# Optimization experiments

Measured on AMD Instinct MI355X. Metric: run time of the kernel, lower is better.

Reference implementation:

```python
import jax, jax.numpy as jnp
import numpy as np

D_MODEL = 256
D_FFN = 1024
N_LEVELS = 4
N_HEADS = 8
N_POINTS = 4
HEAD_DIM = D_MODEL // N_HEADS
SPATIAL = [(128, 128), (64, 64), (32, 32), (16, 16)]
LQ = sum(h * w for h, w in SPATIAL)  # 21760
B = 2


def setup_inputs() -> dict:
    key = jax.random.key(0)
    ks = jax.random.split(key, 24)

    def w(k, shape, s=0.02):
        return (jax.random.normal(k, shape) * s).astype(jnp.float32)

    HLP = N_HEADS * N_LEVELS * N_POINTS
    starts = np.cumsum([0] + [h * w_ for h, w_ in SPATIAL[:-1]])
    return {
        "src": jax.random.normal(ks[0], (B, LQ, D_MODEL), jnp.float32),
        "pos": 0.1 * jax.random.normal(ks[1], (B, LQ, D_MODEL), jnp.float32),
        "reference_points": jax.random.uniform(ks[2], (B, LQ, N_LEVELS, 2), jnp.float32),
        "W_off": w(ks[3], (D_MODEL, HLP * 2)),
        "b_off": w(ks[4], (HLP * 2,), 0.5),
        "W_attn": w(ks[5], (D_MODEL, HLP)),
        "b_attn": jnp.zeros((HLP,), jnp.float32),
        "W_val": w(ks[6], (D_MODEL, D_MODEL)),
        "b_val": jnp.zeros((D_MODEL,), jnp.float32),
        "W_out": w(ks[7], (D_MODEL, D_MODEL)),
        "b_out": jnp.zeros((D_MODEL,), jnp.float32),
        "ln1_g": jnp.ones((D_MODEL,), jnp.float32),
        "ln1_b": jnp.zeros((D_MODEL,), jnp.float32),
        "W1": w(ks[8], (D_MODEL, D_FFN)),
        "b1": jnp.zeros((D_FFN,), jnp.float32),
        "W2": w(ks[9], (D_FFN, D_MODEL)),
        "b2": jnp.zeros((D_MODEL,), jnp.float32),
        "ln2_g": jnp.ones((D_MODEL,), jnp.float32),
        "ln2_b": jnp.zeros((D_MODEL,), jnp.float32),
        "spatial_shapes": np.array(SPATIAL, np.int32),
        "level_start_index": np.array(starts, np.int32),
    }


def _layernorm(x, g, b):
    mu = x.mean(-1, keepdims=True)
    var = ((x - mu) ** 2).mean(-1, keepdims=True)
    return (x - mu) * jax.lax.rsqrt(var + 1e-5) * g + b


def _bilinear_sample(v, x, y, H, W):
    # v: [N, H, W, D]; x, y: [N, Lq, P] pixel coords (align_corners=False, zero pad)
    x0f = jnp.floor(x)
    y0f = jnp.floor(y)
    x0 = x0f.astype(jnp.int32)
    y0 = y0f.astype(jnp.int32)
    wx1 = x - x0f
    wy1 = y - y0f
    wx0 = 1.0 - wx1
    wy0 = 1.0 - wy1
    vf = v.reshape(v.shape[0], H * W, v.shape[-1])

    def gather(xi, yi, wt):
        valid = (xi >= 0) & (xi < W) & (yi >= 0) & (yi < H)
        idx = jnp.clip(yi, 0, H - 1) * W + jnp.clip(xi, 0, W - 1)
        g = jnp.take_along_axis(vf, idx.reshape(idx.shape[0], -1)[..., None], axis=1)
        g = g.reshape(*xi.shape, vf.shape[-1])
        return g * (wt * valid.astype(wt.dtype))[..., None]

    return (gather(x0, y0, wx0 * wy0) + gather(x0 + 1, y0, wx1 * wy0)
            + gather(x0, y0 + 1, wx0 * wy1) + gather(x0 + 1, y0 + 1, wx1 * wy1))


def _ms_deform_attn(query, src, reference_points, W_off, b_off, W_attn, b_attn,
                    W_val, b_val, W_out, b_out, spatial_shapes):
    Bq, Lq, _ = query.shape
    ss = np.asarray(spatial_shapes)
    value = (src @ W_val + b_val).reshape(Bq, Lq, N_HEADS, HEAD_DIM)
    off = (query @ W_off + b_off).reshape(Bq, Lq, N_HEADS, N_LEVELS, N_POINTS, 2)
    attn = (query @ W_attn + b_attn).reshape(Bq, Lq, N_HEADS, N_LEVELS * N_POINTS)
    attn = jax.nn.softmax(attn, axis=-1).reshape(Bq, Lq, N_HEADS, N_LEVELS, N_POINTS)
    # offset normalizer = (W, H) per level
    normalizer = jnp.asarray(ss[:, ::-1].astype(np.float32))  # [L, 2]
    loc = reference_points[:, :, None, :, None, :] + off / normalizer[None, None, None, :, None, :]
    # loc: [B, Lq, M, L, P, 2] normalized in [0,1]
    out = jnp.zeros((Bq, N_HEADS, Lq, HEAD_DIM), query.dtype)
    start = 0
    for lvl in range(N_LEVELS):
        H, W = int(ss[lvl, 0]), int(ss[lvl, 1])
        v = value[:, start:start + H * W]                                 # [B, HW, M, D]
        v = v.transpose(0, 2, 1, 3).reshape(Bq * N_HEADS, H, W, HEAD_DIM)
        l = loc[:, :, :, lvl]                                             # [B, Lq, M, P, 2]
        x = (l[..., 0] * W - 0.5).transpose(0, 2, 1, 3).reshape(Bq * N_HEADS, Lq, N_POINTS)
        y = (l[..., 1] * H - 0.5).transpose(0, 2, 1, 3).reshape(Bq * N_HEADS, Lq, N_POINTS)
        sampled = _bilinear_sample(v, x, y, H, W)                         # [BM, Lq, P, D]
        wgt = attn[:, :, :, lvl].transpose(0, 2, 1, 3).reshape(Bq * N_HEADS, Lq, N_POINTS)
        out = out + (sampled * wgt[..., None]).sum(2).reshape(Bq, N_HEADS, Lq, HEAD_DIM)
        start += H * W
    out = out.transpose(0, 2, 1, 3).reshape(Bq, Lq, D_MODEL)
    return out @ W_out + b_out


def reference(src, pos, reference_points, W_off, b_off, W_attn, b_attn, W_val, b_val,
              W_out, b_out, ln1_g, ln1_b, W1, b1, W2, b2, ln2_g, ln2_b,
              spatial_shapes, level_start_index):
    query = src + pos
    src2 = _ms_deform_attn(query, src, reference_points, W_off, b_off, W_attn, b_attn,
                           W_val, b_val, W_out, b_out, spatial_shapes)
    h = _layernorm(src + src2, ln1_g, ln1_b)
    ffn = jax.nn.relu(h @ W1 + b1) @ W2 + b2
    return _layernorm(h + ffn, ln2_g, ln2_b)
```

## Files before the change

kernel.cpp:

```cpp
#include <hip/hip_runtime.h>

typedef __bf16 bf16x8 __attribute__((ext_vector_type(8)));
typedef float f32x4 __attribute__((ext_vector_type(4)));

static constexpr int TOKS = 43520;
static constexpr int LQN  = 21760;

__device__ __forceinline__ unsigned short f2bf(float f) {
  union { float f; unsigned u; } v; v.f = f;
  return (unsigned short)((v.u + 0x7fffu + ((v.u >> 16) & 1u)) >> 16);
}
__device__ __forceinline__ float bf2f(unsigned short b) {
  union { unsigned u; float f; } v; v.u = ((unsigned)b) << 16; return v.f;
}

__global__ __launch_bounds__(256) void wt6_kernel(
    const float* __restrict__ W_val, const float* __restrict__ W_off,
    const float* __restrict__ W_attn, const float* __restrict__ W_out,
    const float* __restrict__ W1, const float* __restrict__ W2,
    const float* __restrict__ b_off, const float* __restrict__ b_attn,
    unsigned short* __restrict__ Wt_val, unsigned short* __restrict__ Wt_oa,
    unsigned short* __restrict__ Wt_out,
    unsigned short* __restrict__ Wt_1, unsigned short* __restrict__ Wt_2,
    float* __restrict__ b_oa) {
  int gid = blockIdx.x * 256 + threadIdx.x;
  if (gid >= 754048) return;
  if (gid >= 753664) {
    int i = gid - 753664;
    b_oa[i] = (i < 256) ? b_off[i] : b_attn[i - 256];
    return;
  }
  const float* W; unsigned short* Wt; int idx, K, nsh;
  if (gid < 65536)       { W = W_val;  Wt = Wt_val;          idx = gid;          K = 256;  nsh = 8;  }
  else if (gid < 131072) { W = W_off;  Wt = Wt_oa;           idx = gid - 65536;  K = 256;  nsh = 8;  }
  else if (gid < 163840) { W = W_attn; Wt = Wt_oa + 65536;   idx = gid - 131072; K = 256;  nsh = 7;  }
  else if (gid < 229376) { W = W_out;  Wt = Wt_out;          idx = gid - 163840; K = 256;  nsh = 8;  }
  else if (gid < 491520) { W = W1;     Wt = Wt_1;            idx = gid - 229376; K = 256;  nsh = 10; }
  else                   { W = W2;     Wt = Wt_2;            idx = gid - 491520; K = 1024; nsh = 8;  }
  int k = idx >> nsh, n = idx & ((1 << nsh) - 1);
  Wt[n * K + k] = f2bf(W[idx]);
}

__global__ __launch_bounds__(256) void prep_kernel(const float4* __restrict__ src,
                                                   const float4* __restrict__ pos,
                                                   ushort4* __restrict__ srcb,
                                                   ushort4* __restrict__ qb) {
  int i = blockIdx.x * 256 + threadIdx.x;
  float4 s = src[i], p = pos[i];
  srcb[i] = make_ushort4(f2bf(s.x), f2bf(s.y), f2bf(s.z), f2bf(s.w));
  qb[i]   = make_ushort4(f2bf(s.x + p.x), f2bf(s.y + p.y), f2bf(s.z + p.z), f2bf(s.w + p.w));
}

__global__ __launch_bounds__(256) void gemm_bt(const unsigned short* __restrict__ A,
                                               const unsigned short* __restrict__ Bt,
                                               const float* __restrict__ bias,
                                               const unsigned short* __restrict__ res,
                                               void* __restrict__ Cp,
                                               int N, int K, int outop) {
  __shared__ unsigned short As[128][40];
  __shared__ unsigned short Bs[128][40];
  const int t = threadIdx.x;
  const int bm = blockIdx.x, bn = blockIdx.y;
  const int wave = t >> 6, lane = t & 63;
  const int wm = (wave & 1) << 6, wn = (wave >> 1) << 6;
  const int lr = lane & 15, lq = lane >> 4;
  const int row0 = t >> 2, cb0 = (t & 3) * 8;
  const int row1 = row0 + 64;
  f32x4 acc[4][4] = {};

  const size_t abase = (size_t)bm * 128 * K;
  const size_t bbase = (size_t)bn * 128 * K;
  for (int k0 = 0; k0 < K; k0 += 32) {
    __syncthreads();
    *(uint4*)&As[row0][cb0] = *(const uint4*)&A[abase + (size_t)row0 * K + k0 + cb0];
    *(uint4*)&As[row1][cb0] = *(const uint4*)&A[abase + (size_t)row1 * K + k0 + cb0];
    *(uint4*)&Bs[row0][cb0] = *(const uint4*)&Bt[bbase + (size_t)row0 * K + k0 + cb0];
    *(uint4*)&Bs[row1][cb0] = *(const uint4*)&Bt[bbase + (size_t)row1 * K + k0 + cb0];
    __syncthreads();
    bf16x8 af[4], bfr[4];
#pragma unroll
    for (int i = 0; i < 4; i++) af[i] = *(const bf16x8*)&As[wm + i * 16 + lr][lq * 8];
#pragma unroll
    for (int j = 0; j < 4; j++) bfr[j] = *(const bf16x8*)&Bs[wn + j * 16 + lr][lq * 8];
#pragma unroll
    for (int i = 0; i < 4; i++)
#pragma unroll
      for (int j = 0; j < 4; j++)
        acc[i][j] = __builtin_amdgcn_mfma_f32_16x16x32_bf16(af[i], bfr[j], acc[i][j], 0, 0, 0);
  }
  const int rb = bm * 128 + wm + lq * 4;
  const int cbase = bn * 128 + wn + lr;
#pragma unroll
  for (int j = 0; j < 4; j++) {
    const int col = cbase + j * 16;
    const float bv = bias[col];
#pragma unroll
    for (int i = 0; i < 4; i++) {
#pragma unroll
      for (int r = 0; r < 4; r++) {
        float v = acc[i][j][r] + bv;
        size_t o = (size_t)(rb + i * 16 + r) * N + col;
        if (outop == 0) ((float*)Cp)[o] = v;
        else if (outop == 1) ((unsigned short*)Cp)[o] = f2bf(v);
        else if (outop == 2) ((unsigned short*)Cp)[o] = f2bf(fmaxf(v, 0.f));
        else ((unsigned short*)Cp)[o] = f2bf(v + bf2f(res[o]));
      }
    }
  }
}

__device__ __forceinline__ void fma8(uint4 v, float w, float* a) {
  const unsigned uu[4] = {v.x, v.y, v.z, v.w};
#pragma unroll
  for (int i = 0; i < 4; i++) {
    union { unsigned u; float f; } lo, hi;
    lo.u = uu[i] << 16;
    hi.u = uu[i] & 0xffff0000u;
    a[2 * i]     += w * lo.f;
    a[2 * i + 1] += w * hi.f;
  }
}

__global__ __launch_bounds__(256) void deform_kernel(const unsigned short* __restrict__ valb,
                                                     const unsigned short* __restrict__ oab,
                                                     const float* __restrict__ refp,
                                                     unsigned short* __restrict__ outb) {
  __shared__ float4 sW[8][8][17];
  __shared__ int4   sI[8][8][17];
  const int t = threadIdx.x;
  const int bid = blockIdx.x;
  const int nb = (bid & 7) * 680 + (bid >> 3);
  const int tok0 = nb * 8;
  const int SD[4] = {128, 64, 32, 16};

  if (t < 64) {
    const int g = t >> 3, h = t & 7;
    const int tok = tok0 + g;
    const unsigned short* lg = oab + (size_t)tok * 384 + 256 + h * 16;
    uint4 lv0 = ((const uint4*)lg)[0];
    uint4 lv1 = ((const uint4*)lg)[1];
    const unsigned lw[8] = {lv0.x, lv0.y, lv0.z, lv0.w, lv1.x, lv1.y, lv1.z, lv1.w};
    float w[16];
#pragma unroll
    for (int i = 0; i < 8; i++) {
      union { unsigned u; float f; } lo, hi;
      lo.u = lw[i] << 16; hi.u = lw[i] & 0xffff0000u;
      w[2 * i] = lo.f; w[2 * i + 1] = hi.f;
    }
    float mx = -1e30f;
#pragma unroll
    for (int i = 0; i < 16; i++) mx = fmaxf(mx, w[i]);
    float s = 0.f;
#pragma unroll
    for (int i = 0; i < 16; i++) { w[i] = __expf(w[i] - mx); s += w[i]; }
    const float inv = 1.f / s;
    const unsigned short* of = oab + (size_t)tok * 384 + h * 32;
    uint4 o0 = ((const uint4*)of)[0], o1 = ((const uint4*)of)[1];
    uint4 o2 = ((const uint4*)of)[2], o3 = ((const uint4*)of)[3];
    const unsigned ow[16] = {o0.x, o0.y, o0.z, o0.w, o1.x, o1.y, o1.z, o1.w,
                             o2.x, o2.y, o2.z, o2.w, o3.x, o3.y, o3.z, o3.w};
    float off[32];
#pragma unroll
    for (int i = 0; i < 16; i++) {
      union { unsigned u; float f; } lo, hi;
      lo.u = ow[i] << 16; hi.u = ow[i] & 0xffff0000u;
      off[2 * i] = lo.f; off[2 * i + 1] = hi.f;
    }
    const float* rp = refp + (size_t)tok * 8;
#pragma unroll
    for (int l = 0; l < 4; l++) {
      const int S = SD[l];
      const float Sf = (float)S;
      const float rx = rp[l * 2 + 0] * Sf - 0.5f;
      const float ry = rp[l * 2 + 1] * Sf - 0.5f;
#pragma unroll
      for (int p = 0; p < 4; p++) {
        const int idx = l * 4 + p;
        const float x = rx + off[l * 8 + p * 2 + 0];
        const float y = ry + off[l * 8 + p * 2 + 1];
        const float aw = w[idx] * inv;
        const float x0f = floorf(x), y0f = floorf(y);
        const int x0 = (int)x0f, y0 = (int)y0f;
        const float fx = x - x0f, fy = y - y0f;
        const bool xin0 = (x0 >= 0) & (x0 < S), xin1 = (x0 + 1 >= 0) & (x0 + 1 < S);
        const bool yin0 = (y0 >= 0) & (y0 < S), yin1 = (y0 + 1 >= 0) & (y0 + 1 < S);
        const int xc0 = min(max(x0, 0), S - 1), xc1 = min(max(x0 + 1, 0), S - 1);
        const int yc0 = min(max(y0, 0), S - 1), yc1 = min(max(y0 + 1, 0), S - 1);
        sW[g][h][idx] = make_float4(aw * (1.f - fx) * (1.f - fy) * (float)(xin0 & yin0),
                                    aw * fx * (1.f - fy)         * (float)(xin1 & yin0),
                                    aw * (1.f - fx) * fy         * (float)(xin0 & yin1),
                                    aw * fx * fy                 * (float)(xin1 & yin1));
        sI[g][h][idx] = make_int4(yc0 * S + xc0, yc0 * S + xc1,
                                  yc1 * S + xc0, yc1 * S + xc1);
      }
    }
  }
  __syncthreads();

  const int g = t >> 5, h = (t >> 2) & 7, dc = t & 3;
  const int tok = tok0 + g;
  const int b = tok / LQN;
  float acc[8] = {0.f, 0.f, 0.f, 0.f, 0.f, 0.f, 0.f, 0.f};
  const int ST[4] = {0, 16384, 20480, 21504};
#pragma unroll
  for (int l = 0; l < 4; l++) {
    const unsigned short* vb = valb + ((size_t)(b * LQN + ST[l])) * 256 + h * 32 + dc * 8;
#pragma unroll
    for (int p = 0; p < 4; p++) {
      float4 W4 = sW[g][h][l * 4 + p];
      int4   I4 = sI[g][h][l * 4 + p];
      uint4 v00 = *(const uint4*)(vb + (size_t)I4.x * 256);
      uint4 v10 = *(const uint4*)(vb + (size_t)I4.y * 256);
      uint4 v01 = *(const uint4*)(vb + (size_t)I4.z * 256);
      uint4 v11 = *(const uint4*)(vb + (size_t)I4.w * 256);
      fma8(v00, W4.x, acc);
      fma8(v10, W4.y, acc);
      fma8(v01, W4.z, acc);
      fma8(v11, W4.w, acc);
    }
  }
  unsigned o[4];
#pragma unroll
  for (int i = 0; i < 4; i++)
    o[i] = (unsigned)f2bf(acc[2 * i]) | ((unsigned)f2bf(acc[2 * i + 1]) << 16);
  *(uint4*)(outb + (size_t)tok * 256 + h * 32 + dc * 8) = make_uint4(o[0], o[1], o[2], o[3]);
}

template <int OUT_F32>
__global__ __launch_bounds__(256) void ln_kernel(const ushort4* __restrict__ in,
                                                 const float* __restrict__ g,
                                                 const float* __restrict__ beta,
                                                 void* __restrict__ outp) {
  const int wv = blockIdx.x * 4 + (threadIdx.x >> 6);
  const int lane = threadIdx.x & 63;
  const size_t idx = (size_t)wv * 64 + lane;
  ushort4 u = in[idx];
  float x0 = bf2f(u.x), x1 = bf2f(u.y), x2 = bf2f(u.z), x3 = bf2f(u.w);
  float sum = x0 + x1 + x2 + x3;
#pragma unroll
  for (int o = 32; o >= 1; o >>= 1) sum += __shfl_xor(sum, o, 64);
  const float mu = sum * (1.f / 256.f);
  float d0 = x0 - mu, d1 = x1 - mu, d2 = x2 - mu, d3 = x3 - mu;
  float ss = d0 * d0 + d1 * d1 + d2 * d2 + d3 * d3;
#pragma unroll
  for (int o = 32; o >= 1; o >>= 1) ss += __shfl_xor(ss, o, 64);
  const float rs = rsqrtf(ss * (1.f / 256.f) + 1e-5f);
  float4 gg = ((const float4*)g)[lane], bb = ((const float4*)beta)[lane];
  float y0 = d0 * rs * gg.x + bb.x;
  float y1 = d1 * rs * gg.y + bb.y;
  float y2 = d2 * rs * gg.z + bb.z;
  float y3 = d3 * rs * gg.w + bb.w;
  if (OUT_F32) ((float4*)outp)[idx] = make_float4(y0, y1, y2, y3);
  else ((ushort4*)outp)[idx] = make_ushort4(f2bf(y0), f2bf(y1), f2bf(y2), f2bf(y3));
}

extern "C" void kernel_launch(void* const* d_in, const int* in_sizes, int n_in,
                              void* d_out, int out_size, void* d_ws, size_t ws_size,
                              hipStream_t stream) {
  (void)in_sizes; (void)n_in; (void)out_size; (void)ws_size;
  const float* src    = (const float*)d_in[0];
  const float* pos    = (const float*)d_in[1];
  const float* refp   = (const float*)d_in[2];
  const float* W_off  = (const float*)d_in[3];
  const float* b_off  = (const float*)d_in[4];
  const float* W_attn = (const float*)d_in[5];
  const float* b_attn = (const float*)d_in[6];
  const float* W_val  = (const float*)d_in[7];
  const float* b_val  = (const float*)d_in[8];
  const float* W_out  = (const float*)d_in[9];
  const float* b_out  = (const float*)d_in[10];
  const float* ln1_g  = (const float*)d_in[11];
  const float* ln1_b  = (const float*)d_in[12];
  const float* W1     = (const float*)d_in[13];
  const float* b1     = (const float*)d_in[14];
  const float* W2     = (const float*)d_in[15];
  const float* b2     = (const float*)d_in[16];
  const float* ln2_g  = (const float*)d_in[17];
  const float* ln2_b  = (const float*)d_in[18];

  char* ws = (char*)d_ws;
  unsigned short* Wt_val = (unsigned short*)ws;
  unsigned short* Wt_oa  = Wt_val + 65536;
  unsigned short* Wt_out = Wt_oa + 98304;
  unsigned short* Wt_1   = Wt_out + 65536;
  unsigned short* Wt_2   = Wt_1 + 262144;
  float*          b_oa   = (float*)(Wt_2 + 262144);
  const size_t WPOOL = 2u * 1024 * 1024;

  const size_t SZ_bf = (size_t)TOKS * 256 * 2;
  const size_t SZ_oa = (size_t)TOKS * 384 * 2;

  unsigned short* srcb = (unsigned short*)(ws + WPOOL);
  unsigned short* qb   = (unsigned short*)(ws + WPOOL + SZ_bf);
  unsigned short* valb = (unsigned short*)(ws + WPOOL + 2 * SZ_bf);
  unsigned short* oab  = (unsigned short*)(ws + WPOOL + 3 * SZ_bf);
  unsigned short* h_bf = (unsigned short*)(ws + WPOOL + 3 * SZ_bf + SZ_oa);
  unsigned short* hb   = (unsigned short*)(ws + WPOOL + 3 * SZ_bf + SZ_oa + SZ_bf);
  unsigned short* attnoutb = qb;
  unsigned short* preLN1b  = valb;
  unsigned short* preLN2b  = valb;

  wt6_kernel<<<2946, 256, 0, stream>>>(W_val, W_off, W_attn, W_out, W1, W2, b_off, b_attn,
                                       Wt_val, Wt_oa, Wt_out, Wt_1, Wt_2, b_oa);

  prep_kernel<<<10880, 256, 0, stream>>>((const float4*)src, (const float4*)pos,
                                         (ushort4*)srcb, (ushort4*)qb);

  gemm_bt<<<dim3(340, 2), 256, 0, stream>>>(srcb, Wt_val, b_val, nullptr, valb, 256, 256, 1);
  gemm_bt<<<dim3(340, 3), 256, 0, stream>>>(qb, Wt_oa, b_oa, nullptr, oab, 384, 256, 1);

  deform_kernel<<<TOKS / 8, 256, 0, stream>>>(valb, oab, refp, attnoutb);

  gemm_bt<<<dim3(340, 2), 256, 0, stream>>>(attnoutb, Wt_out, b_out, srcb, preLN1b, 256, 256, 3);
  ln_kernel<0><<<10880, 256, 0, stream>>>((const ushort4*)preLN1b, ln1_g, ln1_b, h_bf);

  gemm_bt<<<dim3(340, 8), 256, 0, stream>>>(h_bf, Wt_1, b1, nullptr, hb, 1024, 256, 2);
  gemm_bt<<<dim3(340, 2), 256, 0, stream>>>(hb, Wt_2, b2, h_bf, preLN2b, 256, 1024, 3);

  ln_kernel<1><<<10880, 256, 0, stream>>>((const ushort4*)preLN2b, ln2_g, ln2_b, d_out);
}
```

Measured before the change: 527.5 us.

## Prefetch GEMM tiles into registers, template GEMMs, merge prep and projection launches

The GEMM is turned into a templated body with compile-time K and output op, and it loads the next K-slice from global memory into registers while the current slice is being computed. Weight transposition is merged with the src/pos bf16 conversion into one launch, and the value and offset/attention projections are merged into one launch. The deform kernel also stores its sample indices as 16-bit values instead of 32-bit to cut shared memory traffic. Together these aim to hide global load latency and reduce launch count, at the cost of higher register pressure in the GEMM.

```diff
diff --git a/kernel.cpp b/kernel.cpp
--- a/kernel.cpp
+++ b/kernel.cpp
@@ -14,7 +14,9 @@
   union { unsigned u; float f; } v; v.u = ((unsigned)b) << 16; return v.f;
 }
 
-__global__ __launch_bounds__(256) void wt6_kernel(
+__global__ __launch_bounds__(256) void prewt_kernel(
+    const float* __restrict__ src, const float* __restrict__ pos,
+    unsigned short* __restrict__ srcb, unsigned short* __restrict__ qb,
     const float* __restrict__ W_val, const float* __restrict__ W_off,
     const float* __restrict__ W_attn, const float* __restrict__ W_out,
     const float* __restrict__ W1, const float* __restrict__ W2,
@@ -23,7 +25,16 @@
     unsigned short* __restrict__ Wt_out,
     unsigned short* __restrict__ Wt_1, unsigned short* __restrict__ Wt_2,
     float* __restrict__ b_oa) {
-  int gid = blockIdx.x * 256 + threadIdx.x;
+  const int bid = blockIdx.x;
+  if (bid < 10880) {
+    int i = bid * 256 + threadIdx.x;
+    float4 s = ((const float4*)src)[i], p = ((const float4*)pos)[i];
+    ((ushort4*)srcb)[i] = make_ushort4(f2bf(s.x), f2bf(s.y), f2bf(s.z), f2bf(s.w));
+    ((ushort4*)qb)[i]   = make_ushort4(f2bf(s.x + p.x), f2bf(s.y + p.y),
+                                       f2bf(s.z + p.z), f2bf(s.w + p.w));
+    return;
+  }
+  int gid = (bid - 10880) * 256 + threadIdx.x;
   if (gid >= 754048) return;
   if (gid >= 753664) {
     int i = gid - 753664;
@@ -41,47 +52,47 @@
   Wt[n * K + k] = f2bf(W[idx]);
 }
 
-__global__ __launch_bounds__(256) void prep_kernel(const float4* __restrict__ src,
-                                                   const float4* __restrict__ pos,
-                                                   ushort4* __restrict__ srcb,
-                                                   ushort4* __restrict__ qb) {
-  int i = blockIdx.x * 256 + threadIdx.x;
-  float4 s = src[i], p = pos[i];
-  srcb[i] = make_ushort4(f2bf(s.x), f2bf(s.y), f2bf(s.z), f2bf(s.w));
-  qb[i]   = make_ushort4(f2bf(s.x + p.x), f2bf(s.y + p.y), f2bf(s.z + p.z), f2bf(s.w + p.w));
-}
-
-__global__ __launch_bounds__(256) void gemm_bt(const unsigned short* __restrict__ A,
-                                               const unsigned short* __restrict__ Bt,
-                                               const float* __restrict__ bias,
-                                               const unsigned short* __restrict__ res,
-                                               void* __restrict__ Cp,
-                                               int N, int K, int outop) {
-  __shared__ unsigned short As[128][40];
-  __shared__ unsigned short Bs[128][40];
+template <int K, int OUTOP>
+__device__ __forceinline__ void gemm_body(unsigned short* __restrict__ As,
+                                          unsigned short* __restrict__ Bs,
+                                          const unsigned short* __restrict__ A,
+                                          const unsigned short* __restrict__ Bt,
+                                          const float* __restrict__ bias,
+                                          const unsigned short* __restrict__ res,
+                                          unsigned short* __restrict__ Cp,
+                                          int N, int bm, int bn) {
   const int t = threadIdx.x;
-  const int bm = blockIdx.x, bn = blockIdx.y;
   const int wave = t >> 6, lane = t & 63;
   const int wm = (wave & 1) << 6, wn = (wave >> 1) << 6;
   const int lr = lane & 15, lq = lane >> 4;
-  const int row0 = t >> 2, cb0 = (t & 3) * 8;
-  const int row1 = row0 + 64;
+  const int row0 = t >> 2, cb0 = (t & 3) << 3;
   f32x4 acc[4][4] = {};
-
-  const size_t abase = (size_t)bm * 128 * K;
-  const size_t bbase = (size_t)bn * 128 * K;
+  const unsigned short* ga = A  + (size_t)(bm * 128 + row0) * K + cb0;
+  const unsigned short* gb = Bt + (size_t)(bn * 128 + row0) * K + cb0;
+  const size_t gs = (size_t)64 * K;
+  uint4 pa0 = *(const uint4*)ga;
+  uint4 pa1 = *(const uint4*)(ga + gs);
+  uint4 pb0 = *(const uint4*)gb;
+  uint4 pb1 = *(const uint4*)(gb + gs);
+#pragma unroll 1
   for (int k0 = 0; k0 < K; k0 += 32) {
     __syncthreads();
-    *(uint4*)&As[row0][cb0] = *(const uint4*)&A[abase + (size_t)row0 * K + k0 + cb0];
-    *(uint4*)&As[row1][cb0] = *(const uint4*)&A[abase + (size_t)row1 * K + k0 + cb0];
-    *(uint4*)&Bs[row0][cb0] = *(const uint4*)&Bt[bbase + (size_t)row0 * K + k0 + cb0];
-    *(uint4*)&Bs[row1][cb0] = *(const uint4*)&Bt[bbase + (size_t)row1 * K + k0 + cb0];
+    *(uint4*)&As[row0 * 40 + cb0] = pa0;
+    *(uint4*)&As[(row0 + 64) * 40 + cb0] = pa1;
+    *(uint4*)&Bs[row0 * 40 + cb0] = pb0;
+    *(uint4*)&Bs[(row0 + 64) * 40 + cb0] = pb1;
     __syncthreads();
+    if (k0 + 32 < K) {
+      pa0 = *(const uint4*)(ga + k0 + 32);
+      pa1 = *(const uint4*)(ga + gs + k0 + 32);
+      pb0 = *(const uint4*)(gb + k0 + 32);
+      pb1 = *(const uint4*)(gb + gs + k0 + 32);
+    }
     bf16x8 af[4], bfr[4];
 #pragma unroll
-    for (int i = 0; i < 4; i++) af[i] = *(const bf16x8*)&As[wm + i * 16 + lr][lq * 8];
-#pragma unroll
-    for (int j = 0; j < 4; j++) bfr[j] = *(const bf16x8*)&Bs[wn + j * 16 + lr][lq * 8];
+    for (int i = 0; i < 4; i++) af[i] = *(const bf16x8*)&As[(wm + i * 16 + lr) * 40 + lq * 8];
+#pragma unroll
+    for (int j = 0; j < 4; j++) bfr[j] = *(const bf16x8*)&Bs[(wn + j * 16 + lr) * 40 + lq * 8];
 #pragma unroll
     for (int i = 0; i < 4; i++)
 #pragma unroll
@@ -100,13 +111,52 @@
       for (int r = 0; r < 4; r++) {
         float v = acc[i][j][r] + bv;
         size_t o = (size_t)(rb + i * 16 + r) * N + col;
-        if (outop == 0) ((float*)Cp)[o] = v;
-        else if (outop == 1) ((unsigned short*)Cp)[o] = f2bf(v);
-        else if (outop == 2) ((unsigned short*)Cp)[o] = f2bf(fmaxf(v, 0.f));
-        else ((unsigned short*)Cp)[o] = f2bf(v + bf2f(res[o]));
+        if (OUTOP == 1) Cp[o] = f2bf(v);
+        else if (OUTOP == 2) Cp[o] = f2bf(fmaxf(v, 0.f));
+        else Cp[o] = f2bf(v + bf2f(res[o]));
       }
     }
   }
+}
+
+__global__ __launch_bounds__(256) void proj_kernel(
+    const unsigned short* __restrict__ srcb, const unsigned short* __restrict__ qb,
+    const unsigned short* __restrict__ Wt_val, const unsigned short* __restrict__ Wt_oa,
+    const float* __restrict__ b_val, const float* __restrict__ b_oa,
+    unsigned short* __restrict__ valb, unsigned short* __restrict__ oab) {
+  __shared__ unsigned short As[128 * 40];
+  __shared__ unsigned short Bs[128 * 40];
+  const int bn = blockIdx.y;
+  if (bn < 2)
+    gemm_body<256, 1>(As, Bs, srcb, Wt_val, b_val, nullptr, valb, 256, blockIdx.x, bn);
+  else
+    gemm_body<256, 1>(As, Bs, qb, Wt_oa, b_oa, nullptr, oab, 384, blockIdx.x, bn - 2);
+}
+
+__global__ __launch_bounds__(256) void gemm_out_kernel(
+    const unsigned short* __restrict__ A, const unsigned short* __restrict__ Bt,
+    const float* __restrict__ bias, const unsigned short* __restrict__ res,
+    unsigned short* __restrict__ C) {
+  __shared__ unsigned short As[128 * 40];
+  __shared__ unsigned short Bs[128 * 40];
+  gemm_body<256, 3>(As, Bs, A, Bt, bias, res, C, 256, blockIdx.x, blockIdx.y);
+}
+
+__global__ __launch_bounds__(256) void gemm_ffn1_kernel(
+    const unsigned short* __restrict__ A, const unsigned short* __restrict__ Bt,
+    const float* __restrict__ bias, unsigned short* __restrict__ C) {
+  __shared__ unsigned short As[128 * 40];
+  __shared__ unsigned short Bs[128 * 40];
+  gemm_body<256, 2>(As, Bs, A, Bt, bias, nullptr, C, 1024, blockIdx.x, blockIdx.y);
+}
+
+__global__ __launch_bounds__(256) void gemm_ffn2_kernel(
+    const unsigned short* __restrict__ A, const unsigned short* __restrict__ Bt,
+    const float* __restrict__ bias, const unsigned short* __restrict__ res,
+    unsigned short* __restrict__ C) {
+  __shared__ unsigned short As[128 * 40];
+  __shared__ unsigned short Bs[128 * 40];
+  gemm_body<1024, 3>(As, Bs, A, Bt, bias, res, C, 256, blockIdx.x, blockIdx.y);
 }
 
 __device__ __forceinline__ void fma8(uint4 v, float w, float* a) {
@@ -125,8 +175,8 @@
                                                      const unsigned short* __restrict__ oab,
                                                      const float* __restrict__ refp,
                                                      unsigned short* __restrict__ outb) {
-  __shared__ float4 sW[8][8][17];
-  __shared__ int4   sI[8][8][17];
+  __shared__ float4  sW[8][8][17];
+  __shared__ ushort4 sI[8][8][17];
   const int t = threadIdx.x;
   const int bid = blockIdx.x;
   const int nb = (bid & 7) * 680 + (bid >> 3);
@@ -190,8 +240,10 @@
                                     aw * fx * (1.f - fy)         * (float)(xin1 & yin0),
                                     aw * (1.f - fx) * fy         * (float)(xin0 & yin1),
                                     aw * fx * fy                 * (float)(xin1 & yin1));
-        sI[g][h][idx] = make_int4(yc0 * S + xc0, yc0 * S + xc1,
-                                  yc1 * S + xc0, yc1 * S + xc1);
+        sI[g][h][idx] = make_ushort4((unsigned short)(yc0 * S + xc0),
+                                     (unsigned short)(yc0 * S + xc1),
+                                     (unsigned short)(yc1 * S + xc0),
+                                     (unsigned short)(yc1 * S + xc1));
       }
     }
   }
@@ -207,8 +259,8 @@
     const unsigned short* vb = valb + ((size_t)(b * LQN + ST[l])) * 256 + h * 32 + dc * 8;
 #pragma unroll
     for (int p = 0; p < 4; p++) {
-      float4 W4 = sW[g][h][l * 4 + p];
-      int4   I4 = sI[g][h][l * 4 + p];
+      float4  W4 = sW[g][h][l * 4 + p];
+      ushort4 I4 = sI[g][h][l * 4 + p];
       uint4 v00 = *(const uint4*)(vb + (size_t)I4.x * 256);
       uint4 v10 = *(const uint4*)(vb + (size_t)I4.y * 256);
       uint4 v01 = *(const uint4*)(vb + (size_t)I4.z * 256);
@@ -300,22 +352,20 @@
   unsigned short* preLN1b  = valb;
   unsigned short* preLN2b  = valb;
 
-  wt6_kernel<<<2946, 256, 0, stream>>>(W_val, W_off, W_attn, W_out, W1, W2, b_off, b_attn,
-                                       Wt_val, Wt_oa, Wt_out, Wt_1, Wt_2, b_oa);
-
-  prep_kernel<<<10880, 256, 0, stream>>>((const float4*)src, (const float4*)pos,
-                                         (ushort4*)srcb, (ushort4*)qb);
-
-  gemm_bt<<<dim3(340, 2), 256, 0, stream>>>(srcb, Wt_val, b_val, nullptr, valb, 256, 256, 1);
-  gemm_bt<<<dim3(340, 3), 256, 0, stream>>>(qb, Wt_oa, b_oa, nullptr, oab, 384, 256, 1);
+  prewt_kernel<<<13826, 256, 0, stream>>>(src, pos, srcb, qb,
+                                          W_val, W_off, W_attn, W_out, W1, W2, b_off, b_attn,
+                                          Wt_val, Wt_oa, Wt_out, Wt_1, Wt_2, b_oa);
+
+  proj_kernel<<<dim3(340, 5), 256, 0, stream>>>(srcb, qb, Wt_val, Wt_oa, b_val, b_oa,
+                                                valb, oab);
 
   deform_kernel<<<TOKS / 8, 256, 0, stream>>>(valb, oab, refp, attnoutb);
 
-  gemm_bt<<<dim3(340, 2), 256, 0, stream>>>(attnoutb, Wt_out, b_out, srcb, preLN1b, 256, 256, 3);
+  gemm_out_kernel<<<dim3(340, 2), 256, 0, stream>>>(attnoutb, Wt_out, b_out, srcb, preLN1b);
   ln_kernel<0><<<10880, 256, 0, stream>>>((const ushort4*)preLN1b, ln1_g, ln1_b, h_bf);
 
-  gemm_bt<<<dim3(340, 8), 256, 0, stream>>>(h_bf, Wt_1, b1, nullptr, hb, 1024, 256, 2);
-  gemm_bt<<<dim3(340, 2), 256, 0, stream>>>(hb, Wt_2, b2, h_bf, preLN2b, 256, 1024, 3);
+  gemm_ffn1_kernel<<<dim3(340, 8), 256, 0, stream>>>(h_bf, Wt_1, b1, hb);
+  gemm_ffn2_kernel<<<dim3(340, 2), 256, 0, stream>>>(hb, Wt_2, b2, h_bf, preLN2b);
 
   ln_kernel<1><<<10880, 256, 0, stream>>>((const ushort4*)preLN2b, ln2_g, ln2_b, d_out);
 }
```

Measured after the change: 441.8 us. -16.2%, faster.
